# Performance work log

Measured on AMD Instinct MI355X. Metric: run time of the kernel, lower is better.

## Reference

```python
import jax, jax.numpy as jnp
import numpy as np

N = 100000       # nodes
E = 3200000      # edges (avg degree 32)
NFEAT = 512
NHID = 256
NCLASS = 64
K = 10
ALPHA = 0.1


def setup_inputs() -> dict:
    key = jax.random.key(0)
    ks = jax.random.split(key, 6)
    x = jax.random.normal(ks[0], (N, NFEAT), dtype=jnp.float32)
    edge_index = jax.random.randint(ks[1], (2, E), 0, N)
    W1 = jax.random.normal(ks[2], (NFEAT, NHID), dtype=jnp.float32) / np.float32(np.sqrt(NFEAT))
    b1 = jnp.zeros((NHID,), jnp.float32)
    W2 = jax.random.normal(ks[3], (NHID, NCLASS), dtype=jnp.float32) / np.float32(np.sqrt(NHID))
    b2 = jnp.zeros((NCLASS,), jnp.float32)
    # PPR init of the K+1 GPR coefficients: alpha*(1-alpha)^k, last = (1-alpha)^K
    kk = jnp.arange(K + 1, dtype=jnp.float32)
    temp = (ALPHA * (1.0 - ALPHA) ** kk).astype(jnp.float32)
    temp = temp.at[-1].set(np.float32((1.0 - ALPHA) ** K))
    return {"x": x, "edge_index": edge_index, "W1": W1, "b1": b1, "W2": W2, "b2": b2, "temp": temp}


def reference(x, edge_index, W1, b1, W2, b2, temp):
    # MLP (dropout is identity in eval mode)
    h = jax.nn.relu(x @ W1 + b1)          # [N, NHID]
    h = h @ W2 + b2                        # [N, NCLASS]

    # gcn_norm with self-loops: D^-1/2 (A+I) D^-1/2
    row, col = edge_index[0], edge_index[1]
    loops = jnp.arange(N, dtype=row.dtype)
    row = jnp.concatenate([row, loops])
    col = jnp.concatenate([col, loops])
    w = jnp.ones(row.shape[0], h.dtype)
    deg = jax.ops.segment_sum(w, col, num_segments=N)
    dis = jnp.where(deg > 0, jax.lax.rsqrt(deg), 0.0)
    norm = dis[row] * w * dis[col]         # [E+N]

    # K-hop GPR propagation: hidden = sum_k temp[k] * A_hat^k h
    hidden = h * temp[0]
    for k in range(K):
        h = jax.ops.segment_sum(norm[:, None] * h[row], col, num_segments=N)
        hidden = hidden + temp[k + 1] * h
    return jax.nn.log_softmax(hidden, axis=1)
```

## Files before the change

kernel.cpp:

```cpp
#include <hip/hip_runtime.h>
#include <math.h>

#define NFEAT 512
#define NHID  256
#define NCLS  64
#define KHOP  10
#define LDSTRIDE 56

typedef __attribute__((ext_vector_type(8))) short short8;
typedef __attribute__((ext_vector_type(4))) float f32x4;

__device__ __forceinline__ unsigned short f2bf(float f) {
    unsigned u = __float_as_uint(f);
    u += 0x7FFFu + ((u >> 16) & 1u);
    return (unsigned short)(u >> 16);
}
__device__ __forceinline__ float bf2f(unsigned short h) {
    return __uint_as_float((unsigned)h << 16);
}

__global__ __launch_bounds__(256) void cast_kernel(const float* __restrict__ src,
                                                   unsigned short* __restrict__ dst, long n)
{
    long i = (long)blockIdx.x * 1024 + (long)threadIdx.x * 4;
    if (i + 3 < n) {
        float4 v = *(const float4*)(src + i);
        dst[i+0] = f2bf(v.x); dst[i+1] = f2bf(v.y);
        dst[i+2] = f2bf(v.z); dst[i+3] = f2bf(v.w);
    } else {
        for (int j = 0; j < 4 && i + j < n; j++) dst[i+j] = f2bf(src[i+j]);
    }
}

__global__ __launch_bounds__(256) void castT_kernel(const float* __restrict__ src,
                                                    unsigned short* __restrict__ dst,
                                                    int K, int N)
{
    int i = blockIdx.x * 256 + threadIdx.x;
    if (i < K * N) {
        int k = i / N, n = i % N;
        dst[(long)n * K + k] = f2bf(src[i]);
    }
}

__global__ __launch_bounds__(256) void mfma_gemm1(
    const unsigned short* __restrict__ A, const unsigned short* __restrict__ BT,
    const float* __restrict__ bias, unsigned short* __restrict__ C, int M)
{
    __shared__ unsigned short As[128 * LDSTRIDE];
    __shared__ unsigned short Bs[128 * LDSTRIDE];
    const int tid = threadIdx.x;
    const int wave = tid >> 6, lane = tid & 63;
    const int quad = lane >> 4, l16 = lane & 15;
    const int wm = wave >> 1, wn = wave & 1;
    const int m0 = blockIdx.x * 128, n0 = blockIdx.y * 128;

    f32x4 acc[4][4] = {};
    const int srow = tid >> 2;
    const int schunk = (tid & 3) * 8;

    for (int k0 = 0; k0 < NFEAT; k0 += 32) {
        #pragma unroll
        for (int i = 0; i < 2; i++) {
            int r = srow + i * 64;
            int rg = m0 + r;
            short8 v = {};
            if (rg < M) v = *(const short8*)(A + (long)rg * NFEAT + k0 + schunk);
            *(short8*)(As + r * LDSTRIDE + schunk) = v;
        }
        #pragma unroll
        for (int i = 0; i < 2; i++) {
            int r = srow + i * 64;
            short8 v = *(const short8*)(BT + (long)(n0 + r) * NFEAT + k0 + schunk);
            *(short8*)(Bs + r * LDSTRIDE + schunk) = v;
        }
        __syncthreads();
        short8 af[4], bfr[4];
        #pragma unroll
        for (int mi = 0; mi < 4; mi++)
            af[mi] = *(const short8*)(As + (wm*64 + mi*16 + l16) * LDSTRIDE + quad*8);
        #pragma unroll
        for (int nj = 0; nj < 4; nj++)
            bfr[nj] = *(const short8*)(Bs + (wn*64 + nj*16 + l16) * LDSTRIDE + quad*8);
        #pragma unroll
        for (int mi = 0; mi < 4; mi++)
            #pragma unroll
            for (int nj = 0; nj < 4; nj++)
                acc[mi][nj] = __builtin_amdgcn_mfma_f32_16x16x32_bf16(af[mi], bfr[nj], acc[mi][nj], 0, 0, 0);
        __syncthreads();
    }

    #pragma unroll
    for (int mi = 0; mi < 4; mi++)
        #pragma unroll
        for (int r = 0; r < 4; r++) {
            int row = m0 + wm*64 + mi*16 + quad*4 + r;
            if (row >= M) continue;
            #pragma unroll
            for (int nj = 0; nj < 4; nj++) {
                int col = n0 + wn*64 + nj*16 + l16;
                float v = acc[mi][nj][r] + bias[col];
                C[(long)row * NHID + col] = f2bf(fmaxf(v, 0.f));
            }
        }
}

__global__ __launch_bounds__(256) void mfma_gemm2(
    const unsigned short* __restrict__ A, const unsigned short* __restrict__ BT,
    const float* __restrict__ bias, unsigned short* __restrict__ S,
    float* __restrict__ hidden, const float* __restrict__ temp,
    const float* __restrict__ dis, int M)
{
    __shared__ unsigned short As[128 * LDSTRIDE];
    __shared__ unsigned short Bs[64 * LDSTRIDE];
    const int tid = threadIdx.x;
    const int wave = tid >> 6, lane = tid & 63;
    const int quad = lane >> 4, l16 = lane & 15;
    const int m0 = blockIdx.x * 128;
    const float t0 = temp[0];

    f32x4 acc[2][4] = {};
    const int srow = tid >> 2;
    const int schunk = (tid & 3) * 8;

    for (int k0 = 0; k0 < NHID; k0 += 32) {
        #pragma unroll
        for (int i = 0; i < 2; i++) {
            int r = srow + i * 64;
            int rg = m0 + r;
            short8 v = {};
            if (rg < M) v = *(const short8*)(A + (long)rg * NHID + k0 + schunk);
            *(short8*)(As + r * LDSTRIDE + schunk) = v;
        }
        {
            short8 v = *(const short8*)(BT + (long)srow * NHID + k0 + schunk);
            *(short8*)(Bs + srow * LDSTRIDE + schunk) = v;
        }
        __syncthreads();
        short8 af[2], bfr[4];
        #pragma unroll
        for (int mi = 0; mi < 2; mi++)
            af[mi] = *(const short8*)(As + (wave*32 + mi*16 + l16) * LDSTRIDE + quad*8);
        #pragma unroll
        for (int nj = 0; nj < 4; nj++)
            bfr[nj] = *(const short8*)(Bs + (nj*16 + l16) * LDSTRIDE + quad*8);
        #pragma unroll
        for (int mi = 0; mi < 2; mi++)
            #pragma unroll
            for (int nj = 0; nj < 4; nj++)
                acc[mi][nj] = __builtin_amdgcn_mfma_f32_16x16x32_bf16(af[mi], bfr[nj], acc[mi][nj], 0, 0, 0);
        __syncthreads();
    }

    #pragma unroll
    for (int mi = 0; mi < 2; mi++)
        #pragma unroll
        for (int r = 0; r < 4; r++) {
            int row = m0 + wave*32 + mi*16 + quad*4 + r;
            if (row >= M) continue;
            float dr = dis[row];
            #pragma unroll
            for (int nj = 0; nj < 4; nj++) {
                int col = nj*16 + l16;
                float v = acc[mi][nj][r] + bias[col];
                long idx = (long)row * NCLS + col;
                S[idx] = f2bf(dr * v);
                hidden[idx] = t0 * v;
            }
        }
}

__global__ void count_kernel(const int* __restrict__ ei, int E, int* __restrict__ cnt)
{
    int e = blockIdx.x * blockDim.x + threadIdx.x;
    if (e < E) atomicAdd(&cnt[ei[E + e]], 1);
}

__global__ void dis_kernel(const int* __restrict__ cnt, float* __restrict__ dis, int Nn)
{
    int v = blockIdx.x * blockDim.x + threadIdx.x;
    if (v < Nn) dis[v] = rsqrtf((float)(cnt[v] + 1));
}

__global__ __launch_bounds__(256) void bsum_kernel(const int* __restrict__ cnt, int n,
                                                   int* __restrict__ bsum)
{
    __shared__ int ws[4];
    int i = blockIdx.x * 256 + threadIdx.x;
    int v = (i < n) ? ((cnt[i] + 7) & ~7) : 0;
    #pragma unroll
    for (int off = 1; off < 64; off <<= 1) v += __shfl_xor(v, off);
    if ((threadIdx.x & 63) == 0) ws[threadIdx.x >> 6] = v;
    __syncthreads();
    if (threadIdx.x == 0) bsum[blockIdx.x] = ws[0] + ws[1] + ws[2] + ws[3];
}

__global__ __launch_bounds__(512) void bscan_kernel(int* __restrict__ bsum, int nb)
{
    __shared__ int buf[512];
    int i = threadIdx.x;
    int v = (i < nb) ? bsum[i] : 0;
    buf[i] = v;
    __syncthreads();
    for (int off = 1; off < 512; off <<= 1) {
        int t = (i >= off) ? buf[i - off] : 0;
        __syncthreads();
        buf[i] += t;
        __syncthreads();
    }
    if (i < nb) bsum[i] = buf[i] - v;
}

__global__ __launch_bounds__(256) void pscan_kernel(const int* __restrict__ cnt, int n,
                                                    const int* __restrict__ bsum,
                                                    int* __restrict__ ptr)
{
    __shared__ int buf[256];
    int i = blockIdx.x * 256 + threadIdx.x;
    int v = (i < n) ? ((cnt[i] + 7) & ~7) : 0;
    buf[threadIdx.x] = v;
    __syncthreads();
    for (int off = 1; off < 256; off <<= 1) {
        int t = (threadIdx.x >= off) ? buf[threadIdx.x - off] : 0;
        __syncthreads();
        buf[threadIdx.x] += t;
        __syncthreads();
    }
    if (i < n) ptr[i] = bsum[blockIdx.x] + buf[threadIdx.x] - v;
    if (i == n - 1) ptr[n] = bsum[blockIdx.x] + buf[threadIdx.x];
}

__global__ void fill_kernel(const int* __restrict__ ei, int E,
                            const int* __restrict__ ptr, int* __restrict__ fill,
                            int* __restrict__ adj)
{
    int e = blockIdx.x * blockDim.x + threadIdx.x;
    if (e >= E) return;
    int r = ei[e];
    int c = ei[E + e];
    int pos = atomicAdd(&fill[c], 1);
    adj[ptr[c] + pos] = r;
}

__global__ void padfill_kernel(const int* __restrict__ cnt, const int* __restrict__ ptr,
                               int* __restrict__ adj, int Nn)
{
    int v = blockIdx.x * 256 + threadIdx.x;
    if (v >= Nn) return;
    int b = ptr[v] + cnt[v], e = ptr[v + 1];
    for (int i = b; i < e; i++) adj[i] = Nn;
}

__global__ void zdum_kernel(unsigned short* __restrict__ sA,
                            unsigned short* __restrict__ sB, int Nn)
{
    int i = threadIdx.x;
    if (i < 64) sA[(long)Nn * NCLS + i] = 0;
    else        sB[(long)Nn * NCLS + (i - 64)] = 0;
}

__global__ __launch_bounds__(256) void prop_kernel(
    const unsigned short* __restrict__ sin, unsigned short* __restrict__ sout,
    float* __restrict__ hidden,
    const int* __restrict__ ptr, const int* __restrict__ adj,
    const float* __restrict__ dis, const float* __restrict__ temp, int k, int Nn)
{
    const int wave = threadIdx.x >> 6, lane = threadIdx.x & 63;
    const int v = blockIdx.x * 4 + wave;
    if (v >= Nn) return;

    const int beg = ptr[v], end = ptr[v + 1];
    const float d = dis[v];
    float acc = bf2f(sin[v * NCLS + lane]);

    for (int e = beg; e < end; e += 8) {
        int4 u0 = *(const int4*)(adj + e);
        int4 u1 = *(const int4*)(adj + e + 4);
        float a0 = bf2f(sin[u0.x * NCLS + lane]);
        float a1 = bf2f(sin[u0.y * NCLS + lane]);
        float a2 = bf2f(sin[u0.z * NCLS + lane]);
        float a3 = bf2f(sin[u0.w * NCLS + lane]);
        float a4 = bf2f(sin[u1.x * NCLS + lane]);
        float a5 = bf2f(sin[u1.y * NCLS + lane]);
        float a6 = bf2f(sin[u1.z * NCLS + lane]);
        float a7 = bf2f(sin[u1.w * NCLS + lane]);
        acc += ((a0 + a1) + (a2 + a3)) + ((a4 + a5) + (a6 + a7));
    }

    int idx = v * NCLS + lane;
    float h = d * acc;
    hidden[idx] += temp[k + 1] * h;
    sout[idx] = f2bf(d * h);
}

__global__ __launch_bounds__(256) void lsm_kernel(const float* __restrict__ hidden,
                                                  float* __restrict__ out, int Nn)
{
    const int wave = threadIdx.x >> 6, lane = threadIdx.x & 63;
    const int v = blockIdx.x * 4 + wave;
    if (v >= Nn) return;
    float x = hidden[(long)v * NCLS + lane];
    float m = x;
    #pragma unroll
    for (int off = 32; off > 0; off >>= 1) m = fmaxf(m, __shfl_xor(m, off));
    float s = __expf(x - m);
    #pragma unroll
    for (int off = 32; off > 0; off >>= 1) s += __shfl_xor(s, off);
    out[(long)v * NCLS + lane] = x - m - logf(s);
}

extern "C" void kernel_launch(void* const* d_in, const int* in_sizes, int n_in,
                              void* d_out, int out_size, void* d_ws, size_t ws_size,
                              hipStream_t stream)
{
    const float* x    = (const float*)d_in[0];
    const int*   ei   = (const int*)  d_in[1];
    const float* W1   = (const float*)d_in[2];
    const float* b1   = (const float*)d_in[3];
    const float* W2   = (const float*)d_in[4];
    const float* b2   = (const float*)d_in[5];
    const float* temp = (const float*)d_in[6];

    const int Nn = in_sizes[0] / NFEAT;
    const int E  = in_sizes[1] / 2;

    char* ws = (char*)d_ws;
    size_t off = 0;
    auto alloc = [&](size_t bytes) { size_t o = off; off += (bytes + 255) & ~255ull; return o; };

    size_t r0 = alloc((size_t)Nn * NFEAT * 2);
    size_t hmid_off = alloc((size_t)Nn * NHID * 2);
    size_t w1t_off  = alloc((size_t)NFEAT * NHID * 2);
    size_t w2t_off  = alloc((size_t)NHID * NCLS * 2);
    size_t cnt_off  = alloc((size_t)Nn * 4);
    size_t fill_off = alloc((size_t)Nn * 4);
    size_t dis_off  = alloc((size_t)Nn * 4);
    size_t ptr_off  = alloc((size_t)(Nn + 1) * 4);
    size_t bsum_off = alloc(((size_t)Nn / 256 + 2) * 4);

    unsigned short* x_bf = (unsigned short*)(ws + r0);
    unsigned short* hmid = (unsigned short*)(ws + hmid_off);
    unsigned short* W1T  = (unsigned short*)(ws + w1t_off);
    unsigned short* W2T  = (unsigned short*)(ws + w2t_off);
    int*   cnt   = (int*)  (ws + cnt_off);
    int*   fillb = (int*)  (ws + fill_off);
    float* dis   = (float*)(ws + dis_off);
    int*   ptr   = (int*)  (ws + ptr_off);
    int*   bsum  = (int*)  (ws + bsum_off);

    size_t Epad = (size_t)E + 8ull * Nn;
    int*            adj    = (int*)           (ws + r0);
    unsigned short* sA     = (unsigned short*)(ws + r0 + Epad * 4);
    unsigned short* sB     = (unsigned short*)(ws + r0 + Epad * 4 + (size_t)(Nn + 1) * NCLS * 2);
    float*          hidden = (float*)         (ws + r0 + Epad * 4 + (size_t)(Nn + 1) * NCLS * 4);

    cast_kernel<<<(int)(((long)Nn * NFEAT + 1023) / 1024), 256, 0, stream>>>(x, x_bf, (long)Nn * NFEAT);
    castT_kernel<<<(NFEAT * NHID + 255) / 256, 256, 0, stream>>>(W1, W1T, NFEAT, NHID);
    castT_kernel<<<(NHID * NCLS + 255) / 256, 256, 0, stream>>>(W2, W2T, NHID, NCLS);

    {
        dim3 g((Nn + 127) / 128, NHID / 128);
        mfma_gemm1<<<g, 256, 0, stream>>>(x_bf, W1T, b1, hmid, Nn);
    }

    hipMemsetAsync(cnt,   0, (size_t)Nn * 4, stream);
    hipMemsetAsync(fillb, 0, (size_t)Nn * 4, stream);
    count_kernel<<<(E + 255) / 256, 256, 0, stream>>>(ei, E, cnt);
    dis_kernel<<<(Nn + 255) / 256, 256, 0, stream>>>(cnt, dis, Nn);
    int nb = (Nn + 255) / 256;
    bsum_kernel<<<nb, 256, 0, stream>>>(cnt, Nn, bsum);
    bscan_kernel<<<1, 512, 0, stream>>>(bsum, nb);
    pscan_kernel<<<nb, 256, 0, stream>>>(cnt, Nn, bsum, ptr);
    fill_kernel<<<(E + 255) / 256, 256, 0, stream>>>(ei, E, ptr, fillb, adj);
    padfill_kernel<<<(Nn + 255) / 256, 256, 0, stream>>>(cnt, ptr, adj, Nn);
    zdum_kernel<<<1, 128, 0, stream>>>(sA, sB, Nn);

    mfma_gemm2<<<(Nn + 127) / 128, 256, 0, stream>>>(hmid, W2T, b2, sA, hidden, temp, dis, Nn);

    int pg = (Nn + 3) / 4;
    for (int k = 0; k < KHOP; k++) {
        const unsigned short* sin = (k & 1) ? sB : sA;
        unsigned short*       so  = (k & 1) ? sA : sB;
        prop_kernel<<<pg, 256, 0, stream>>>(sin, so, hidden, ptr, adj, dis, temp, k, Nn);
    }

    lsm_kernel<<<pg, 256, 0, stream>>>(hidden, (float*)d_out, Nn);
}
```

Baseline: 1.418 ms.

## Fuse x bf16 cast into GEMM1 and partition CSR fill by XCD

Removes the separate fp32-to-bf16 cast pass over x by converting it inside the first GEMM's tile loads. GEMM1 now uses 64x256 tiles, so each block covers all hidden columns and reads x only once. The CSR fill kernel is restructured so each block handles a chunk of edges but only those whose destination falls in the node range of one of 8 XCD partitions. This is meant to keep atomics and adjacency writes local to one XCD's L2, at the cost of every edge column being read 8 times. The workspace layout is reorganized since the x_bf buffer is no longer needed.

```diff
diff --git a/kernel.cpp b/kernel.cpp
--- a/kernel.cpp
+++ b/kernel.cpp
@@ -6,6 +6,8 @@
 #define NCLS  64
 #define KHOP  10
 #define LDSTRIDE 56
+#define NXCD 8
+#define FCHUNK 8192
 
 typedef __attribute__((ext_vector_type(8))) short short8;
 typedef __attribute__((ext_vector_type(4))) float f32x4;
@@ -19,19 +21,6 @@
     return __uint_as_float((unsigned)h << 16);
 }
 
-__global__ __launch_bounds__(256) void cast_kernel(const float* __restrict__ src,
-                                                   unsigned short* __restrict__ dst, long n)
-{
-    long i = (long)blockIdx.x * 1024 + (long)threadIdx.x * 4;
-    if (i + 3 < n) {
-        float4 v = *(const float4*)(src + i);
-        dst[i+0] = f2bf(v.x); dst[i+1] = f2bf(v.y);
-        dst[i+2] = f2bf(v.z); dst[i+3] = f2bf(v.w);
-    } else {
-        for (int j = 0; j < 4 && i + j < n; j++) dst[i+j] = f2bf(src[i+j]);
-    }
-}
-
 __global__ __launch_bounds__(256) void castT_kernel(const float* __restrict__ src,
                                                     unsigned short* __restrict__ dst,
                                                     int K, int N)
@@ -43,45 +32,50 @@
     }
 }
 
-__global__ __launch_bounds__(256) void mfma_gemm1(
-    const unsigned short* __restrict__ A, const unsigned short* __restrict__ BT,
+__global__ __launch_bounds__(256) void mfma_gemm1_f32(
+    const float* __restrict__ A, const unsigned short* __restrict__ BT,
     const float* __restrict__ bias, unsigned short* __restrict__ C, int M)
 {
-    __shared__ unsigned short As[128 * LDSTRIDE];
-    __shared__ unsigned short Bs[128 * LDSTRIDE];
+    __shared__ unsigned short As[64 * LDSTRIDE];
+    __shared__ unsigned short Bs[256 * LDSTRIDE];
     const int tid = threadIdx.x;
     const int wave = tid >> 6, lane = tid & 63;
     const int quad = lane >> 4, l16 = lane & 15;
-    const int wm = wave >> 1, wn = wave & 1;
-    const int m0 = blockIdx.x * 128, n0 = blockIdx.y * 128;
+    const int m0 = blockIdx.x * 64;
 
     f32x4 acc[4][4] = {};
     const int srow = tid >> 2;
     const int schunk = (tid & 3) * 8;
 
     for (int k0 = 0; k0 < NFEAT; k0 += 32) {
-        #pragma unroll
-        for (int i = 0; i < 2; i++) {
+        {
+            int rg = m0 + srow;
+            short8 v = {};
+            if (rg < M) {
+                const float* p = A + (long)rg * NFEAT + k0 + schunk;
+                float4 f0 = *(const float4*)p;
+                float4 f1 = *(const float4*)(p + 4);
+                v[0] = (short)f2bf(f0.x); v[1] = (short)f2bf(f0.y);
+                v[2] = (short)f2bf(f0.z); v[3] = (short)f2bf(f0.w);
+                v[4] = (short)f2bf(f1.x); v[5] = (short)f2bf(f1.y);
+                v[6] = (short)f2bf(f1.z); v[7] = (short)f2bf(f1.w);
+            }
+            *(short8*)(As + srow * LDSTRIDE + schunk) = v;
+        }
+        #pragma unroll
+        for (int i = 0; i < 4; i++) {
             int r = srow + i * 64;
-            int rg = m0 + r;
-            short8 v = {};
-            if (rg < M) v = *(const short8*)(A + (long)rg * NFEAT + k0 + schunk);
-            *(short8*)(As + r * LDSTRIDE + schunk) = v;
-        }
-        #pragma unroll
-        for (int i = 0; i < 2; i++) {
-            int r = srow + i * 64;
-            short8 v = *(const short8*)(BT + (long)(n0 + r) * NFEAT + k0 + schunk);
+            short8 v = *(const short8*)(BT + (long)r * NFEAT + k0 + schunk);
             *(short8*)(Bs + r * LDSTRIDE + schunk) = v;
         }
         __syncthreads();
         short8 af[4], bfr[4];
         #pragma unroll
         for (int mi = 0; mi < 4; mi++)
-            af[mi] = *(const short8*)(As + (wm*64 + mi*16 + l16) * LDSTRIDE + quad*8);
+            af[mi] = *(const short8*)(As + (mi*16 + l16) * LDSTRIDE + quad*8);
         #pragma unroll
         for (int nj = 0; nj < 4; nj++)
-            bfr[nj] = *(const short8*)(Bs + (wn*64 + nj*16 + l16) * LDSTRIDE + quad*8);
+            bfr[nj] = *(const short8*)(Bs + (wave*64 + nj*16 + l16) * LDSTRIDE + quad*8);
         #pragma unroll
         for (int mi = 0; mi < 4; mi++)
             #pragma unroll
@@ -94,11 +88,11 @@
     for (int mi = 0; mi < 4; mi++)
         #pragma unroll
         for (int r = 0; r < 4; r++) {
-            int row = m0 + wm*64 + mi*16 + quad*4 + r;
+            int row = m0 + mi*16 + quad*4 + r;
             if (row >= M) continue;
             #pragma unroll
             for (int nj = 0; nj < 4; nj++) {
-                int col = n0 + wn*64 + nj*16 + l16;
+                int col = wave*64 + nj*16 + l16;
                 float v = acc[mi][nj][r] + bias[col];
                 C[(long)row * NHID + col] = f2bf(fmaxf(v, 0.f));
             }
@@ -230,16 +224,26 @@
     if (i == n - 1) ptr[n] = bsum[blockIdx.x] + buf[threadIdx.x];
 }
 
-__global__ void fill_kernel(const int* __restrict__ ei, int E,
-                            const int* __restrict__ ptr, int* __restrict__ fill,
-                            int* __restrict__ adj)
-{
-    int e = blockIdx.x * blockDim.x + threadIdx.x;
-    if (e >= E) return;
-    int r = ei[e];
-    int c = ei[E + e];
-    int pos = atomicAdd(&fill[c], 1);
-    adj[ptr[c] + pos] = r;
+__global__ __launch_bounds__(256) void fill2_kernel(const int* __restrict__ ei, int E, int Nn,
+                                                    const int* __restrict__ ptr,
+                                                    int* __restrict__ fill,
+                                                    int* __restrict__ adj)
+{
+    const int s     = blockIdx.x & (NXCD - 1);
+    const int chunk = blockIdx.x >> 3;
+    const int lo = (int)(((long)s * Nn) / NXCD);
+    const int hi = (int)(((long)(s + 1) * Nn) / NXCD);
+    const int base = chunk * FCHUNK;
+    int lim = base + FCHUNK; if (lim > E) lim = E;
+    const int* colp = ei + E;
+    for (int e0 = base + threadIdx.x * 4; e0 < lim; e0 += 1024) {
+        int4 c4 = *(const int4*)(colp + e0);
+        int c;
+        c = c4.x; if (c >= lo && c < hi) { int r = ei[e0];     int p = atomicAdd(&fill[c], 1); adj[ptr[c] + p] = r; }
+        c = c4.y; if (c >= lo && c < hi) { int r = ei[e0 + 1]; int p = atomicAdd(&fill[c], 1); adj[ptr[c] + p] = r; }
+        c = c4.z; if (c >= lo && c < hi) { int r = ei[e0 + 2]; int p = atomicAdd(&fill[c], 1); adj[ptr[c] + p] = r; }
+        c = c4.w; if (c >= lo && c < hi) { int r = ei[e0 + 3]; int p = atomicAdd(&fill[c], 1); adj[ptr[c] + p] = r; }
+    }
 }
 
 __global__ void padfill_kernel(const int* __restrict__ cnt, const int* __restrict__ ptr,
@@ -328,40 +332,24 @@
     size_t off = 0;
     auto alloc = [&](size_t bytes) { size_t o = off; off += (bytes + 255) & ~255ull; return o; };
 
-    size_t r0 = alloc((size_t)Nn * NFEAT * 2);
-    size_t hmid_off = alloc((size_t)Nn * NHID * 2);
-    size_t w1t_off  = alloc((size_t)NFEAT * NHID * 2);
-    size_t w2t_off  = alloc((size_t)NHID * NCLS * 2);
-    size_t cnt_off  = alloc((size_t)Nn * 4);
-    size_t fill_off = alloc((size_t)Nn * 4);
-    size_t dis_off  = alloc((size_t)Nn * 4);
-    size_t ptr_off  = alloc((size_t)(Nn + 1) * 4);
-    size_t bsum_off = alloc(((size_t)Nn / 256 + 2) * 4);
-
-    unsigned short* x_bf = (unsigned short*)(ws + r0);
-    unsigned short* hmid = (unsigned short*)(ws + hmid_off);
-    unsigned short* W1T  = (unsigned short*)(ws + w1t_off);
-    unsigned short* W2T  = (unsigned short*)(ws + w2t_off);
-    int*   cnt   = (int*)  (ws + cnt_off);
-    int*   fillb = (int*)  (ws + fill_off);
-    float* dis   = (float*)(ws + dis_off);
-    int*   ptr   = (int*)  (ws + ptr_off);
-    int*   bsum  = (int*)  (ws + bsum_off);
-
     size_t Epad = (size_t)E + 8ull * Nn;
-    int*            adj    = (int*)           (ws + r0);
-    unsigned short* sA     = (unsigned short*)(ws + r0 + Epad * 4);
-    unsigned short* sB     = (unsigned short*)(ws + r0 + Epad * 4 + (size_t)(Nn + 1) * NCLS * 2);
-    float*          hidden = (float*)         (ws + r0 + Epad * 4 + (size_t)(Nn + 1) * NCLS * 4);
-
-    cast_kernel<<<(int)(((long)Nn * NFEAT + 1023) / 1024), 256, 0, stream>>>(x, x_bf, (long)Nn * NFEAT);
+    int*            adj    = (int*)           (ws + alloc(Epad * 4));
+    unsigned short* sA     = (unsigned short*)(ws + alloc((size_t)(Nn + 1) * NCLS * 2));
+    unsigned short* sB     = (unsigned short*)(ws + alloc((size_t)(Nn + 1) * NCLS * 2));
+    float*          hidden = (float*)         (ws + alloc((size_t)Nn * NCLS * 4));
+    unsigned short* hmid   = (unsigned short*)(ws + alloc((size_t)Nn * NHID * 2));
+    unsigned short* W1T    = (unsigned short*)(ws + alloc((size_t)NFEAT * NHID * 2));
+    unsigned short* W2T    = (unsigned short*)(ws + alloc((size_t)NHID * NCLS * 2));
+    int*   cnt   = (int*)  (ws + alloc((size_t)Nn * 4));
+    int*   fillb = (int*)  (ws + alloc((size_t)Nn * 4));
+    float* dis   = (float*)(ws + alloc((size_t)Nn * 4));
+    int*   ptr   = (int*)  (ws + alloc((size_t)(Nn + 1) * 4));
+    int*   bsum  = (int*)  (ws + alloc(((size_t)Nn / 256 + 2) * 4));
+
     castT_kernel<<<(NFEAT * NHID + 255) / 256, 256, 0, stream>>>(W1, W1T, NFEAT, NHID);
     castT_kernel<<<(NHID * NCLS + 255) / 256, 256, 0, stream>>>(W2, W2T, NHID, NCLS);
 
-    {
-        dim3 g((Nn + 127) / 128, NHID / 128);
-        mfma_gemm1<<<g, 256, 0, stream>>>(x_bf, W1T, b1, hmid, Nn);
-    }
+    mfma_gemm1_f32<<<(Nn + 63) / 64, 256, 0, stream>>>(x, W1T, b1, hmid, Nn);
 
     hipMemsetAsync(cnt,   0, (size_t)Nn * 4, stream);
     hipMemsetAsync(fillb, 0, (size_t)Nn * 4, stream);
@@ -371,7 +359,8 @@
     bsum_kernel<<<nb, 256, 0, stream>>>(cnt, Nn, bsum);
     bscan_kernel<<<1, 512, 0, stream>>>(bsum, nb);
     pscan_kernel<<<nb, 256, 0, stream>>>(cnt, Nn, bsum, ptr);
-    fill_kernel<<<(E + 255) / 256, 256, 0, stream>>>(ei, E, ptr, fillb, adj);
+    int nch = (E + FCHUNK - 1) / FCHUNK;
+    fill2_kernel<<<nch * NXCD, 256, 0, stream>>>(ei, E, Nn, ptr, fillb, adj);
     padfill_kernel<<<(Nn + 255) / 256, 256, 0, stream>>>(cnt, ptr, adj, Nn);
     zdum_kernel<<<1, 128, 0, stream>>>(sA, sB, Nn);
 
```

Result: faster. 1.365 ms (-3.7%).
